# Kernel tuning notes

Measured on AMD Instinct MI355X. Metric: run time of the kernel, lower is better.

## Reference

```python
import jax, jax.numpy as jnp
import numpy as np

K = 3        # deform kernel size
PAD = 1      # autopad(3)
STRIDE = 1

def _conv2d(x, w, b, stride, pad):
    out = jax.lax.conv_general_dilated(
        x, w, (stride, stride), [(pad, pad), (pad, pad)],
        dimension_numbers=('NCHW', 'OIHW', 'NCHW'))
    return out + b[None, :, None, None]

def setup_inputs() -> dict:
    key = jax.random.key(0)
    k1, k2, k3 = jax.random.split(key, 3)
    B, C1, C2, H, W = 16, 128, 128, 80, 80
    x = jax.random.normal(k1, (B, C1, H, W), dtype=jnp.float32)
    # offset-predicting conv: 2*K*K output channels, 3x3 kernel
    offset_w = jax.random.normal(k2, (2 * K * K, C1, 3, 3), dtype=jnp.float32) * 0.05
    offset_b = jnp.zeros((2 * K * K,), dtype=jnp.float32)
    fan_in = C1 * K * K
    weight = jax.random.normal(k3, (C2, C1, K, K), dtype=jnp.float32) * (1.0 / np.sqrt(fan_in))
    bias = jnp.zeros((C2,), dtype=jnp.float32)
    return {'x': x, 'offset_w': offset_w, 'offset_b': offset_b,
            'weight': weight, 'bias': bias}

def _deform_conv(x, offset, weight, bias):
    # x: [B,C,H,W]; offset: [B,2*K*K,Ho,Wo] in (dy,dx) pairs per kernel tap
    B, C, H, W = x.shape
    c2 = weight.shape[0]
    Ho, Wo = offset.shape[2], offset.shape[3]
    off = offset.reshape(B, K * K, 2, Ho, Wo)
    dy, dx = off[:, :, 0], off[:, :, 1]             # [B,KK,Ho,Wo]
    ii, jj = jnp.meshgrid(jnp.arange(K), jnp.arange(K), indexing='ij')
    ki = ii.reshape(-1).astype(jnp.float32)          # [KK]
    kj = jj.reshape(-1).astype(jnp.float32)
    hg = (jnp.arange(Ho) * STRIDE - PAD).astype(jnp.float32)
    wg = (jnp.arange(Wo) * STRIDE - PAD).astype(jnp.float32)
    py = hg[None, None, :, None] + ki[None, :, None, None] + dy  # [B,KK,Ho,Wo]
    px = wg[None, None, None, :] + kj[None, :, None, None] + dx
    y0 = jnp.floor(py); x0 = jnp.floor(px)
    wy1 = py - y0; wy0 = 1.0 - wy1
    wx1 = px - x0; wx0 = 1.0 - wx1

    def corner(yc, xc, wgt):
        valid = (yc >= 0) & (yc < H) & (xc >= 0) & (xc < W)
        yi = jnp.clip(yc, 0, H - 1).astype(jnp.int32)
        xi = jnp.clip(xc, 0, W - 1).astype(jnp.int32)
        # gather per batch: [B,C,KK,Ho,Wo]
        v = jax.vmap(lambda xb, yb, xb2: xb[:, yb, xb2])(x, yi, xi)
        return v * (wgt * valid.astype(x.dtype))[:, None]

    sampled = (corner(y0, x0, wy0 * wx0) + corner(y0, x0 + 1, wy0 * wx1)
               + corner(y0 + 1, x0, wy1 * wx0) + corner(y0 + 1, x0 + 1, wy1 * wx1))
    # grouped weighted sum (g=1): weight [c2, C, K, K] -> [c2, C, KK]
    out = jnp.einsum('bcphw,ocp->bohw', sampled, weight.reshape(c2, C, K * K))
    return out + bias[None, :, None, None]

def reference(x, offset_w, offset_b, weight, bias):
    offset = _conv2d(x, offset_w, offset_b, STRIDE, 1)  # [B, 2*K*K, Ho, Wo]
    return _deform_conv(x, offset, weight, bias)
```

## Files before the change

### kernel.cpp

```cpp
#include <hip/hip_runtime.h>

#define HH 80
#define WW 80
#define C1 128
#define C2 128
#define NB 16
#define HWSZ 6400
#define KKT 1152

typedef __attribute__((ext_vector_type(8))) short bf16x8;
typedef __attribute__((ext_vector_type(4))) float f32x4;

union PkU   { uint4 v; uint d[4]; bf16x8 h; };
union CornU { uint4 v; uint d[4]; };

__device__ inline ushort f2bf(float f) {
  unsigned u = __float_as_uint(f);
  return (ushort)((u + 0x7FFFu + ((u >> 16) & 1u)) >> 16);
}

__device__ inline uint cvtpk(float lo, float hi) {
  uint r;
  asm("v_cvt_pk_bf16_f32 %0, %1, %2" : "=v"(r) : "v"(lo), "v"(hi));
  return r;
}
__device__ inline float bfu_lo(uint w) { return __uint_as_float(w << 16); }
__device__ inline float bfu_hi(uint w) { return __uint_as_float(w & 0xFFFF0000u); }

__device__ inline void gload_lds16(const ushort* g, ushort* l) {
  __builtin_amdgcn_global_load_lds(
      (const __attribute__((address_space(1))) void*)g,
      (__attribute__((address_space(3))) void*)l, 16, 0, 0);
}

__global__ __launch_bounds__(256) void xpose_prep_kernel(
    const float* __restrict__ x, ushort* __restrict__ xt,
    const float* __restrict__ w, const float* __restrict__ ow,
    ushort* __restrict__ wbf, ushort* __restrict__ wobf) {
  __shared__ float ts[64][65];
  const int idx = blockIdx.x;
  const int tid = threadIdx.x;

  if (idx < 3200) {
    const int b = idx / 200;
    const int rem = idx % 200;
    const int c0 = (rem / 100) * 64;
    const int hw0 = (rem % 100) * 64;
    const int lane = tid & 63;

    #pragma unroll
    for (int it = 0; it < 16; it++) {
      int cl = (tid >> 6) + it * 4;
      ts[cl][lane] = x[((size_t)(b * C1 + c0 + cl)) * HWSZ + hw0 + lane];
    }
    __syncthreads();

    #pragma unroll
    for (int it = 0; it < 2; it++) {
      int u = tid + it * 256;
      int j = u >> 3, cg = u & 7;
      CornU pk;
      #pragma unroll
      for (int m = 0; m < 4; m++)
        pk.d[m] = cvtpk(ts[cg * 8 + 2 * m][j], ts[cg * 8 + 2 * m + 1][j]);
      *(uint4*)(xt + ((size_t)b * HWSZ + hw0 + j) * C1 + c0 + cg * 8) = pk.v;
    }
  } else {
    int o = (idx - 3200) * 256 + tid;
    if (o < C2 * KKT) {
      int j  = o & 7;
      int ch = (o >> 3) & 127;
      int kt = o >> 12;
      int kg = (o >> 10) & 3;
      int kprime = kt * 32 + kg * 8 + j;
      int p = kprime >> 7;
      int c = kprime & 127;
      wbf[o] = f2bf(w[(size_t)ch * KKT + c * 9 + p]);
    } else {
      int o2 = o - C2 * KKT;
      int j  = o2 & 7;
      int ch = (o2 >> 3) & 31;
      int kt = o2 >> 10;
      int kg = (o2 >> 8) & 3;
      int kprime = kt * 32 + kg * 8 + j;
      int p = kprime >> 7;
      int c = kprime & 127;
      wobf[o2] = (ch < 18) ? f2bf(ow[(size_t)ch * KKT + c * 9 + p]) : (ushort)0;
    }
  }
}

__global__ __launch_bounds__(256) void offset_mfma_kernel(
    const ushort* __restrict__ xt, const ushort* __restrict__ wobf,
    const float* __restrict__ ob, float* __restrict__ offs) {
  const int bid = blockIdx.x;
  const int b = bid & 15;
  const int tile = bid >> 4;
  const int h0 = (tile / 5) * 4;
  const int w0 = (tile % 5) * 16;
  const int tid = threadIdx.x;
  const int lane = tid & 63;
  const int wave = tid >> 6;
  const int pl = lane & 15, cg = lane >> 4;
  const int spos = wave * 16 + pl;

  __shared__ ushort s_t[4][64][8];
  __shared__ ushort w_t[4][32][8];

  f32x4 acc0 = {0.f, 0.f, 0.f, 0.f}, acc1 = {0.f, 0.f, 0.f, 0.f};
  const ushort* xtb = xt + (size_t)b * HWSZ * C1;

  auto shifted_load = [&](int kt) -> uint4 {
    const int p = kt >> 2, c0 = (kt & 3) << 5;
    const int row = h0 + (spos >> 4) + (p / 3) - 1;
    const int col = w0 + (spos & 15) + (p % 3) - 1;
    uint4 v = {0u, 0u, 0u, 0u};
    if ((unsigned)row < (unsigned)HH && (unsigned)col < (unsigned)WW)
      v = *(const uint4*)(xtb + ((size_t)row * WW + col) * C1 + c0 + cg * 8);
    return v;
  };

  uint4 cv = shifted_load(0);
  uint4 cw = {0u, 0u, 0u, 0u};
  if (tid < 128) cw = ((const uint4*)wobf)[tid];

  #pragma unroll 4
  for (int kt = 0; kt < 36; ++kt) {
    uint4 nv = {0u, 0u, 0u, 0u}, nw = {0u, 0u, 0u, 0u};
    if (kt < 35) {
      nv = shifted_load(kt + 1);
      if (tid < 128) nw = ((const uint4*)(wobf + (size_t)(kt + 1) * 1024))[tid];
    }

    __syncthreads();
    ((uint4*)s_t)[cg * 64 + spos] = cv;
    if (tid < 128) ((uint4*)w_t)[tid] = cw;
    __syncthreads();

    const int q = lane >> 4, c15 = lane & 15;
    bf16x8 bfrag = *(const bf16x8*)&s_t[q][wave * 16 + c15][0];
    bf16x8 a0 = *(const bf16x8*)&w_t[q][c15][0];
    bf16x8 a1 = *(const bf16x8*)&w_t[q][16 + c15][0];
    acc0 = __builtin_amdgcn_mfma_f32_16x16x32_bf16(a0, bfrag, acc0, 0, 0, 0);
    acc1 = __builtin_amdgcn_mfma_f32_16x16x32_bf16(a1, bfrag, acc1, 0, 0, 0);

    cv = nv; cw = nw;
  }

  {
    const int q = lane >> 4, c15 = lane & 15;
    const int ho = h0 + wave, wo = w0 + c15;
    #pragma unroll
    for (int r = 0; r < 4; r++) {
      int ch = q * 4 + r;
      if (ch < 18)
        offs[((size_t)b * 18 + ch) * HWSZ + ho * WW + wo] = acc0[r] + ob[ch];
      int ch1 = 16 + q * 4 + r;
      if (ch1 < 18)
        offs[((size_t)b * 18 + ch1) * HWSZ + ho * WW + wo] = acc1[r] + ob[ch1];
    }
  }
}

struct Geo { float f00, f01, f10, f11; int o00, o01, o10, o11; };

__device__ inline Geo make_geo(float4 cd) {
  Geo g;
  int y0 = (int)cd.x, x0 = (int)cd.y;
  float wy1 = cd.z, wx1 = cd.w;
  float fy0 = ((unsigned)y0 < (unsigned)HH) ? (1.f - wy1) : 0.f;
  float fy1 = ((unsigned)(y0 + 1) < (unsigned)HH) ? wy1 : 0.f;
  float fx0 = ((unsigned)x0 < (unsigned)WW) ? (1.f - wx1) : 0.f;
  float fx1 = ((unsigned)(x0 + 1) < (unsigned)WW) ? wx1 : 0.f;
  g.f00 = fy0 * fx0; g.f01 = fy0 * fx1;
  g.f10 = fy1 * fx0; g.f11 = fy1 * fx1;
  int r0 = min(max(y0, 0), HH - 1), r1 = min(max(y0 + 1, 0), HH - 1);
  int q0 = min(max(x0, 0), WW - 1), q1 = min(max(x0 + 1, 0), WW - 1);
  g.o00 = (r0 * WW + q0) * C1; g.o01 = (r0 * WW + q1) * C1;
  g.o10 = (r1 * WW + q0) * C1; g.o11 = (r1 * WW + q1) * C1;
  return g;
}

__global__ __launch_bounds__(256) void dconv_mfma_kernel(
    const ushort* __restrict__ xt, const float* __restrict__ offs,
    const ushort* __restrict__ wbf, const float* __restrict__ bias,
    float* __restrict__ out) {
  const int bid = blockIdx.x;
  const int b = bid & 15;
  const int tile = bid >> 4;
  const int h0 = (tile / 5) * 4;
  const int w0 = (tile % 5) * 16;
  const int tid = threadIdx.x;
  const int lane = tid & 63;
  const int wave = tid >> 6;
  const int q = lane >> 4, c15 = lane & 15;
  const int spos = wave * 16 + c15;

  __shared__ float4 crd[9][64];
  __shared__ ushort w_pbuf[4][4096];
  __shared__ ushort smp[4][16][128];

  const ushort* xtb = xt + (size_t)b * HWSZ * C1;

  {
    const int ho = h0 + wave, wo = w0 + c15;
    const float* obp = offs + (size_t)b * 18 * HWSZ + ho * WW + wo;
    #pragma unroll
    for (int p = 0; p < 9; ++p) {
      if ((p & 3) == q) {
        float dy = obp[(size_t)(2 * p) * HWSZ];
        float dx = obp[(size_t)(2 * p + 1) * HWSZ];
        float py = (float)(ho - 1 + p / 3) + dy;
        float px = (float)(wo - 1 + p % 3) + dx;
        float y0f = floorf(py), x0f = floorf(px);
        crd[p][spos] = make_float4(y0f, x0f, py - y0f, px - x0f);
      }
    }
  }

  const int jp = lane >> 4;
  const int s  = lane & 15;

  float4 fw[4];
  uint4  cr[4][4];

  auto issue_p = [&](int p) {
    #pragma unroll
    for (int jj = 0; jj < 4; ++jj) {
      Geo gg = make_geo(crd[p][wave * 16 + 4 * jj + jp]);
      fw[jj] = make_float4(gg.f00, gg.f01, gg.f10, gg.f11);
      const ushort* cp = xtb + s * 8;
      cr[jj][0] = *(const uint4*)(cp + gg.o00);
      cr[jj][1] = *(const uint4*)(cp + gg.o01);
      cr[jj][2] = *(const uint4*)(cp + gg.o10);
      cr[jj][3] = *(const uint4*)(cp + gg.o11);
    }
  };

  auto stage_p = [&](int p) {
    #pragma unroll
    for (int j = 0; j < 8; ++j)
      gload_lds16(wbf + ((size_t)(4 * p + wave)) * 4096 + (j * 64 + lane) * 8,
                  w_pbuf[wave] + j * 512);
  };

  auto bilinear_write = [&]() {
    #pragma unroll
    for (int jj = 0; jj < 4; ++jj) {
      const int pos = 4 * jj + jp;
      CornU u0, u1, u2, u3;
      PkU pk;
      u0.v = cr[jj][0]; u1.v = cr[jj][1]; u2.v = cr[jj][2]; u3.v = cr[jj][3];
      const float f00 = fw[jj].x, f01 = fw[jj].y, f10 = fw[jj].z, f11 = fw[jj].w;
      #pragma unroll
      for (int d = 0; d < 4; ++d) {
        float ol = f00 * bfu_lo(u0.d[d]);
        float oh = f00 * bfu_hi(u0.d[d]);
        ol = fmaf(f01, bfu_lo(u1.d[d]), ol);
        oh = fmaf(f01, bfu_hi(u1.d[d]), oh);
        ol = fmaf(f10, bfu_lo(u2.d[d]), ol);
        oh = fmaf(f10, bfu_hi(u2.d[d]), oh);
        ol = fmaf(f11, bfu_lo(u3.d[d]), ol);
        oh = fmaf(f11, bfu_hi(u3.d[d]), oh);
        pk.d[d] = cvtpk(ol, oh);
      }
      char* wp = (char*)&smp[wave][pos][0] + ((s * 16) ^ ((pos & 7) << 4));
      *(uint4*)wp = pk.v;
    }
  };

  f32x4 acc[8];
  #pragma unroll
  for (int mt = 0; mt < 8; mt++) acc[mt] = (f32x4){0.f, 0.f, 0.f, 0.f};

  issue_p(0);
  asm volatile("" ::: "memory");

  #pragma unroll 1
  for (int p = 0; p < 9; ++p) {
    asm volatile("s_waitcnt lgkmcnt(0)" ::: "memory");
    __builtin_amdgcn_s_barrier();

    stage_p(p);
    asm volatile("" ::: "memory");

    bilinear_write();

    if (p < 8) {
      issue_p(p + 1);
      asm volatile("" ::: "memory");
      asm volatile("s_waitcnt vmcnt(16)" ::: "memory");
    } else {
      asm volatile("s_waitcnt vmcnt(0)" ::: "memory");
    }
    __builtin_amdgcn_sched_barrier(0);
    asm volatile("s_waitcnt lgkmcnt(0)" ::: "memory");
    __builtin_amdgcn_s_barrier();

    #pragma unroll
    for (int kk = 0; kk < 4; ++kk) {
      const char* bp = (const char*)&smp[wave][c15][0] +
                       ((kk * 64 + q * 16) ^ ((c15 & 7) << 4));
      bf16x8 bfrag = *(const bf16x8*)bp;
      #pragma unroll
      for (int mt = 0; mt < 8; mt++) {
        bf16x8 afrag = *(const bf16x8*)&w_pbuf[kk][(q * 128 + mt * 16 + c15) * 8];
        acc[mt] = __builtin_amdgcn_mfma_f32_16x16x32_bf16(afrag, bfrag, acc[mt], 0, 0, 0);
      }
    }
  }

  {
    const int ho = h0 + wave, wo = w0 + c15;
    #pragma unroll
    for (int mt = 0; mt < 8; mt++) {
      #pragma unroll
      for (int r = 0; r < 4; r++) {
        int ch = mt * 16 + q * 4 + r;
        out[((size_t)b * C2 + ch) * HWSZ + ho * WW + wo] = acc[mt][r] + bias[ch];
      }
    }
  }
}

extern "C" void kernel_launch(void* const* d_in, const int* in_sizes, int n_in,
                              void* d_out, int out_size, void* d_ws, size_t ws_size,
                              hipStream_t stream) {
  const float* x    = (const float*)d_in[0];
  const float* ow   = (const float*)d_in[1];
  const float* ob   = (const float*)d_in[2];
  const float* wgt  = (const float*)d_in[3];
  const float* bias = (const float*)d_in[4];
  float* out = (float*)d_out;

  ushort* xt   = (ushort*)d_ws;
  float*  offs = (float*)((char*)d_ws + 26214400);
  ushort* wbf  = (ushort*)((char*)d_ws + 26214400 + 7372800);
  ushort* wobf = (ushort*)((char*)d_ws + 26214400 + 7372800 + 294912);

  xpose_prep_kernel<<<dim3(3920), dim3(256), 0, stream>>>(x, xt, wgt, ow, wbf, wobf);
  offset_mfma_kernel<<<dim3(1600), dim3(256), 0, stream>>>(xt, wobf, ob, offs);
  dconv_mfma_kernel<<<dim3(1600), dim3(256), 0, stream>>>(xt, offs, wbf, bias, out);
}
```

Baseline: 236.6 us.

## Stage offset-conv operands via direct global-to-LDS loads with swizzled layout

Rewrites the offset conv kernel's main loop to iterate over the 9 kernel taps. Each tap loads all 128 channels of the shifted input and the matching weight slice straight into LDS using global_load_lds, in place of register staging across 36 small k-steps. Out-of-bounds pixels point at a zeroed pad buffer written by the prep kernel, and an XOR swizzle on the LDS layout is meant to avoid bank conflicts. This cuts barrier count and register traffic, but the loads are no longer overlapped with MFMA, since each tap waits on vmcnt(0).

```diff
diff --git a/kernel.cpp b/kernel.cpp
--- a/kernel.cpp
+++ b/kernel.cpp
@@ -36,7 +36,8 @@
 __global__ __launch_bounds__(256) void xpose_prep_kernel(
     const float* __restrict__ x, ushort* __restrict__ xt,
     const float* __restrict__ w, const float* __restrict__ ow,
-    ushort* __restrict__ wbf, ushort* __restrict__ wobf) {
+    ushort* __restrict__ wbf, ushort* __restrict__ wobf,
+    ushort* __restrict__ zpad) {
   __shared__ float ts[64][65];
   const int idx = blockIdx.x;
   const int tid = threadIdx.x;
@@ -66,6 +67,10 @@
       *(uint4*)(xt + ((size_t)b * HWSZ + hw0 + j) * C1 + c0 + cg * 8) = pk.v;
     }
   } else {
+    if (idx == 3200 && tid < 16) {
+      uint4 z = {0u, 0u, 0u, 0u};
+      ((uint4*)zpad)[tid] = z;
+    }
     int o = (idx - 3200) * 256 + tid;
     if (o < C2 * KKT) {
       int j  = o & 7;
@@ -92,7 +97,8 @@
 
 __global__ __launch_bounds__(256) void offset_mfma_kernel(
     const ushort* __restrict__ xt, const ushort* __restrict__ wobf,
-    const float* __restrict__ ob, float* __restrict__ offs) {
+    const ushort* __restrict__ zpad, const float* __restrict__ ob,
+    float* __restrict__ offs) {
   const int bid = blockIdx.x;
   const int b = bid & 15;
   const int tile = bid >> 4;
@@ -101,54 +107,54 @@
   const int tid = threadIdx.x;
   const int lane = tid & 63;
   const int wave = tid >> 6;
-  const int pl = lane & 15, cg = lane >> 4;
-  const int spos = wave * 16 + pl;
-
-  __shared__ ushort s_t[4][64][8];
-  __shared__ ushort w_t[4][32][8];
-
+  const int q = lane >> 4, c15 = lane & 15;
+
+  __shared__ ushort w_obuf[4][1024];
+  __shared__ ushort smp[4][16][128];
+
+  const ushort* xtb = xt + (size_t)b * HWSZ * C1;
   f32x4 acc0 = {0.f, 0.f, 0.f, 0.f}, acc1 = {0.f, 0.f, 0.f, 0.f};
-  const ushort* xtb = xt + (size_t)b * HWSZ * C1;
-
-  auto shifted_load = [&](int kt) -> uint4 {
-    const int p = kt >> 2, c0 = (kt & 3) << 5;
-    const int row = h0 + (spos >> 4) + (p / 3) - 1;
-    const int col = w0 + (spos & 15) + (p % 3) - 1;
-    uint4 v = {0u, 0u, 0u, 0u};
-    if ((unsigned)row < (unsigned)HH && (unsigned)col < (unsigned)WW)
-      v = *(const uint4*)(xtb + ((size_t)row * WW + col) * C1 + c0 + cg * 8);
-    return v;
-  };
-
-  uint4 cv = shifted_load(0);
-  uint4 cw = {0u, 0u, 0u, 0u};
-  if (tid < 128) cw = ((const uint4*)wobf)[tid];
-
-  #pragma unroll 4
-  for (int kt = 0; kt < 36; ++kt) {
-    uint4 nv = {0u, 0u, 0u, 0u}, nw = {0u, 0u, 0u, 0u};
-    if (kt < 35) {
-      nv = shifted_load(kt + 1);
-      if (tid < 128) nw = ((const uint4*)(wobf + (size_t)(kt + 1) * 1024))[tid];
-    }
-
-    __syncthreads();
-    ((uint4*)s_t)[cg * 64 + spos] = cv;
-    if (tid < 128) ((uint4*)w_t)[tid] = cw;
-    __syncthreads();
-
-    const int q = lane >> 4, c15 = lane & 15;
-    bf16x8 bfrag = *(const bf16x8*)&s_t[q][wave * 16 + c15][0];
-    bf16x8 a0 = *(const bf16x8*)&w_t[q][c15][0];
-    bf16x8 a1 = *(const bf16x8*)&w_t[q][16 + c15][0];
-    acc0 = __builtin_amdgcn_mfma_f32_16x16x32_bf16(a0, bfrag, acc0, 0, 0, 0);
-    acc1 = __builtin_amdgcn_mfma_f32_16x16x32_bf16(a1, bfrag, acc1, 0, 0, 0);
-
-    cv = nv; cw = nw;
+
+  #pragma unroll 1
+  for (int p = 0; p < 9; ++p) {
+    asm volatile("s_waitcnt lgkmcnt(0)" ::: "memory");
+    __builtin_amdgcn_s_barrier();
+
+    #pragma unroll
+    for (int j = 0; j < 2; ++j)
+      gload_lds16(wobf + (size_t)(4 * p + wave) * 1024 + (j * 64 + lane) * 8,
+                  &w_obuf[wave][j * 512]);
+
+    {
+      const int row = h0 + wave + p / 3 - 1;
+      #pragma unroll
+      for (int jj = 0; jj < 4; ++jj) {
+        const int pos = 4 * jj + q;
+        const int col = w0 + pos + p % 3 - 1;
+        const int sl = c15 ^ (pos & 7);
+        const ushort* src =
+            ((unsigned)row < (unsigned)HH && (unsigned)col < (unsigned)WW)
+                ? xtb + ((size_t)row * WW + col) * C1 + sl * 8
+                : zpad + sl * 8;
+        gload_lds16(src, &smp[wave][4 * jj][0]);
+      }
+    }
+
+    asm volatile("s_waitcnt vmcnt(0)" ::: "memory");
+    __builtin_amdgcn_s_barrier();
+
+    #pragma unroll
+    for (int kk = 0; kk < 4; ++kk) {
+      bf16x8 bfrag = *(const bf16x8*)
+          &smp[wave][c15][(((4 * kk + q) ^ (c15 & 7)) * 8)];
+      bf16x8 a0 = *(const bf16x8*)&w_obuf[kk][(q * 32 + c15) * 8];
+      bf16x8 a1 = *(const bf16x8*)&w_obuf[kk][(q * 32 + 16 + c15) * 8];
+      acc0 = __builtin_amdgcn_mfma_f32_16x16x32_bf16(a0, bfrag, acc0, 0, 0, 0);
+      acc1 = __builtin_amdgcn_mfma_f32_16x16x32_bf16(a1, bfrag, acc1, 0, 0, 0);
+    }
   }
 
   {
-    const int q = lane >> 4, c15 = lane & 15;
     const int ho = h0 + wave, wo = w0 + c15;
     #pragma unroll
     for (int r = 0; r < 4; r++) {
@@ -337,8 +343,9 @@
   float*  offs = (float*)((char*)d_ws + 26214400);
   ushort* wbf  = (ushort*)((char*)d_ws + 26214400 + 7372800);
   ushort* wobf = (ushort*)((char*)d_ws + 26214400 + 7372800 + 294912);
-
-  xpose_prep_kernel<<<dim3(3920), dim3(256), 0, stream>>>(x, xt, wgt, ow, wbf, wobf);
-  offset_mfma_kernel<<<dim3(1600), dim3(256), 0, stream>>>(xt, wobf, ob, offs);
+  ushort* zpad = (ushort*)((char*)d_ws + 26214400 + 7372800 + 294912 + 73728);
+
+  xpose_prep_kernel<<<dim3(3920), dim3(256), 0, stream>>>(x, xt, wgt, ow, wbf, wobf, zpad);
+  offset_mfma_kernel<<<dim3(1600), dim3(256), 0, stream>>>(xt, wobf, zpad, ob, offs);
   dconv_mfma_kernel<<<dim3(1600), dim3(256), 0, stream>>>(xt, offs, wbf, bias, out);
 }
```

After: 219.8 us. -7.1%, faster.
